# Performance work log

Measured on AMD Instinct MI355X. Metric: run time of the kernel, lower is better.

Reference implementation:

```python
import jax, jax.numpy as jnp
import numpy as np

B, S, H = 8, 1024, 1024
NH, HD = 16, 64
LN_EPS = 1e-12


def setup_inputs() -> dict:
    key = jax.random.key(0)
    ks = jax.random.split(key, 8)
    sd = 0.02
    return {
        "hidden_states": jax.random.normal(ks[0], (B, S, H), jnp.float32),
        "attention_mask": jnp.zeros((B, 1, 1, S), jnp.float32),
        "Wq": jax.random.normal(ks[1], (H, H), jnp.float32) * sd,
        "bq": jnp.zeros((H,), jnp.float32),
        "Wk": jax.random.normal(ks[2], (H, H), jnp.float32) * sd,
        "bk": jnp.zeros((H,), jnp.float32),
        "Wv": jax.random.normal(ks[3], (H, H), jnp.float32) * sd,
        "bv": jnp.zeros((H,), jnp.float32),
        "Wo": jax.random.normal(ks[4], (H, H), jnp.float32) * sd,
        "bo": jnp.zeros((H,), jnp.float32),
        "ln_gamma": jnp.ones((H,), jnp.float32),
        "ln_beta": jnp.zeros((H,), jnp.float32),
    }


def _heads(x):
    # [B,S,H] -> [B,NH,S,HD]
    return x.reshape(B, S, NH, HD).transpose(0, 2, 1, 3)


def reference(hidden_states, attention_mask, Wq, bq, Wk, bk, Wv, bv, Wo, bo, ln_gamma, ln_beta):
    # QKV projections (torch Linear: x @ W.T + b)
    q = _heads(hidden_states @ Wq.T + bq)
    k = _heads(hidden_states @ Wk.T + bk)
    v = _heads(hidden_states @ Wv.T + bv)
    # scaled dot-product attention with additive mask
    scores = jnp.einsum("bhqd,bhkd->bhqk", q, k) / np.sqrt(HD).astype(np.float32)
    scores = scores + attention_mask  # broadcast [B,1,1,S]
    probs = jax.nn.softmax(scores, axis=-1)
    ctx = jnp.einsum("bhqk,bhkd->bhqd", probs, v)
    ctx = ctx.transpose(0, 2, 1, 3).reshape(B, S, H)
    # output projection + residual + LayerNorm
    out = ctx @ Wo.T + bo
    x = out + hidden_states
    mu = jnp.mean(x, axis=-1, keepdims=True)
    var = jnp.var(x, axis=-1, keepdims=True)
    return (x - mu) * jax.lax.rsqrt(var + LN_EPS) * ln_gamma + ln_beta
```

## Files before the change

kernel.cpp:

```cpp
#include <hip/hip_runtime.h>
#include <stdint.h>

typedef __attribute__((ext_vector_type(8))) __bf16 bf16x8;
typedef __attribute__((ext_vector_type(8))) unsigned short ushortx8;
typedef __attribute__((ext_vector_type(4))) unsigned short ushortx4;
typedef __attribute__((ext_vector_type(4))) short short4v;
typedef __attribute__((ext_vector_type(4))) float floatx4;

#define LOG2E 1.4426950408889634f
#define QSCALE 0.18033688011112043f

#define ASYNC16(g, l) __builtin_amdgcn_global_load_lds( \
    (__attribute__((address_space(1))) void*)(g),       \
    (__attribute__((address_space(3))) void*)(l), 16, 0, 0)

__device__ __forceinline__ unsigned short f2bf(float f) {
    unsigned int u = __float_as_uint(f);
    u += 0x7fffu + ((u >> 16) & 1u);
    return (unsigned short)(u >> 16);
}
__device__ __forceinline__ float bf2f(unsigned short u) {
    return __uint_as_float((unsigned)u << 16);
}

__device__ __forceinline__ floatx4 mfma32(bf16x8 a, bf16x8 b, floatx4 c) {
    return __builtin_amdgcn_mfma_f32_16x16x32_bf16(a, b, c, 0, 0, 0);
}
__device__ __forceinline__ floatx4 mfma16(short4v a, short4v b, floatx4 c) {
    return __builtin_amdgcn_mfma_f32_16x16x16bf16_1k(a, b, c, 0, 0, 0);
}

__global__ __launch_bounds__(256) void cvt_all(
    const float* __restrict__ hidden,
    const float* __restrict__ Wq, const float* __restrict__ Wk,
    const float* __restrict__ Wv, const float* __restrict__ Wo,
    unsigned short* __restrict__ hid_bf,
    unsigned short* __restrict__ oqkv, unsigned short* __restrict__ oo)
{
    const float* src;
    unsigned short* dst;
    int i;
    if (blockIdx.x < 4096) {
        src = hidden; dst = hid_bf;
        i = blockIdx.x * 256 + threadIdx.x;
    } else {
        int blk = (blockIdx.x - 4096) >> 9;
        src = (blk == 0) ? Wq : (blk == 1) ? Wk : (blk == 2) ? Wv : Wo;
        dst = (blk == 3) ? oo : oqkv + (size_t)blk * 1048576;
        i = ((blockIdx.x - 4096) & 511) * 256 + threadIdx.x;
    }
    const float4* p = (const float4*)src + (size_t)i * 2;
    float4 a = p[0], b = p[1];
    ushortx8 o;
    o[0] = f2bf(a.x); o[1] = f2bf(a.y); o[2] = f2bf(a.z); o[3] = f2bf(a.w);
    o[4] = f2bf(b.x); o[5] = f2bf(b.y); o[6] = f2bf(b.z); o[7] = f2bf(b.w);
    *((ushortx8*)dst + i) = o;
}

template<bool SWAP>
__device__ __forceinline__ void kloop_bk64(
    const unsigned short* __restrict__ Ag,
    const unsigned short* __restrict__ Wg,
    unsigned short* As, unsigned short* Bs,
    int wm, int wn, int l16, int quad, int t,
    floatx4 acc[4][4])
{
#pragma unroll 1
    for (int k0 = 0; k0 < 1024; k0 += 64) {
        __syncthreads();
#pragma unroll
        for (int i = 0; i < 4; i++) {
            ASYNC16(Ag + (size_t)i * 32 * 1024 + k0, As + i * 2048 + t * 8);
            ASYNC16(Wg + (size_t)i * 32 * 1024 + k0, Bs + i * 2048 + t * 8);
        }
        __syncthreads();
#pragma unroll
        for (int s = 0; s < 2; s++) {
            int pb = ((s * 4 + quad) ^ (l16 & 7)) * 8;
            bf16x8 af[4], bfr[4];
#pragma unroll
            for (int mt = 0; mt < 4; mt++)
                af[mt] = *(const bf16x8*)(As + (wm + mt * 16 + l16) * 64 + pb);
#pragma unroll
            for (int nt = 0; nt < 4; nt++)
                bfr[nt] = *(const bf16x8*)(Bs + (wn + nt * 16 + l16) * 64 + pb);
            if (SWAP) {
#pragma unroll
                for (int ft = 0; ft < 4; ft++)
#pragma unroll
                    for (int st = 0; st < 4; st++)
                        acc[ft][st] = mfma32(bfr[ft], af[st], acc[ft][st]);
            } else {
#pragma unroll
                for (int mt = 0; mt < 4; mt++)
#pragma unroll
                    for (int nt = 0; nt < 4; nt++)
                        acc[mt][nt] = mfma32(af[mt], bfr[nt], acc[mt][nt]);
            }
        }
    }
}

__global__ __launch_bounds__(256) void gemm_qkv(
    const unsigned short* __restrict__ A,
    const unsigned short* __restrict__ W,
    const float* __restrict__ bq, const float* __restrict__ bk, const float* __restrict__ bv,
    unsigned short* __restrict__ Qo, unsigned short* __restrict__ Ko,
    unsigned short* __restrict__ Vo)
{
    __shared__ unsigned short As[128 * 64];
    __shared__ unsigned short Bs[128 * 64];
    const int t = threadIdx.x;
    const int wave = t >> 6, lane = t & 63;
    const int quad = lane >> 4, l16 = lane & 15;
    const int wm = (wave >> 1) * 64, wn = (wave & 1) * 64;
    const int srow = t >> 3;
    const int scol = ((t & 7) ^ (srow & 7)) * 8;

    const unsigned short* Ag = A + ((size_t)blockIdx.x * 128 + srow) * 1024 + scol;
    const unsigned short* Wg = W + ((size_t)blockIdx.y * 128 + srow) * 1024 + scol;

    floatx4 acc[4][4] = {};
    kloop_bk64<true>(Ag, Wg, As, Bs, wm, wn, l16, quad, t, acc);

    int y = blockIdx.y;
    if (y < 16) {
        const float* bp = (y < 8) ? bq : bk;
        unsigned short* op = (y < 8) ? Qo : Ko;
        float sc = (y < 8) ? QSCALE : 1.0f;
#pragma unroll
        for (int ft = 0; ft < 4; ft++) {
            int featg = (y * 128 + wn + ft * 16 + quad * 4) & 1023;
            float4 b4 = *(const float4*)(bp + featg);
            int h = featg >> 6, d = featg & 63;
#pragma unroll
            for (int st = 0; st < 4; st++) {
                int sg = blockIdx.x * 128 + wm + st * 16 + l16;
                int b = sg >> 10, s = sg & 1023;
                ushortx4 o4;
                o4[0] = f2bf((acc[ft][st][0] + b4.x) * sc);
                o4[1] = f2bf((acc[ft][st][1] + b4.y) * sc);
                o4[2] = f2bf((acc[ft][st][2] + b4.z) * sc);
                o4[3] = f2bf((acc[ft][st][3] + b4.w) * sc);
                *(ushortx4*)(op + (((size_t)(b * 16 + h) * 1024 + s) * 64 + d)) = o4;
            }
        }
    } else {
#pragma unroll
        for (int ft = 0; ft < 4; ft++) {
            int featg = (y * 128 + wn + ft * 16 + quad * 4) & 1023;
            float4 b4 = *(const float4*)(bv + featg);
#pragma unroll
            for (int r = 0; r < 4; r++) {
                int feat = featg + r;
                int h = feat >> 6, d = feat & 63;
                float bias = (r == 0) ? b4.x : (r == 1) ? b4.y : (r == 2) ? b4.z : b4.w;
#pragma unroll
                for (int st = 0; st < 4; st++) {
                    int sg = blockIdx.x * 128 + wm + st * 16 + l16;
                    int b = sg >> 10, s = sg & 1023;
                    int sp = (s & ~63) + (st >> 1) * 32 + (l16 >> 2) * 8 + (st & 1) * 4 + (l16 & 3);
                    Vo[((size_t)(b * 16 + h) * 64 + d) * 1024 + sp] = f2bf(acc[ft][st][r] + bias);
                }
            }
        }
    }
}

__global__ __launch_bounds__(256) void attn(
    const unsigned short* __restrict__ Q,
    const unsigned short* __restrict__ Kg,
    const unsigned short* __restrict__ Vt,
    const float* __restrict__ mask,
    unsigned short* __restrict__ ctx)
{
    __shared__ unsigned short Ks[64 * 64];
    __shared__ unsigned short Vs[64 * 64];
    __shared__ float Msall[1024];

    const int t = threadIdx.x;
    const int wave = t >> 6, lane = t & 63, quad = lane >> 4, l16 = lane & 15;
    const int s7 = l16 & 7;
    const int head = blockIdx.x;
    const int b = head >> 4, h = head & 15;
    const int q0 = blockIdx.y * 128;
    const unsigned short* Qh = Q + (size_t)head * 65536;
    const unsigned short* Kh = Kg + (size_t)head * 65536;
    const unsigned short* Vh = Vt + (size_t)head * 65536;

    const int srow = t >> 3;
    const int scol = ((t & 7) ^ (srow & 7)) * 8;

    {
        float4 m4 = *(const float4*)(mask + b * 1024 + t * 4);
        m4.x *= LOG2E; m4.y *= LOG2E; m4.z *= LOG2E; m4.w *= LOG2E;
        *(float4*)(Msall + t * 4) = m4;
    }

    bf16x8 qf[2][2];
#pragma unroll
    for (int qg = 0; qg < 2; qg++) {
        const unsigned short* qp = Qh + (size_t)(q0 + wave * 32 + qg * 16 + l16) * 64 + quad * 8;
        qf[qg][0] = *(const bf16x8*)(qp);
        qf[qg][1] = *(const bf16x8*)(qp + 32);
    }

    float rs0 = 0.f, rs1 = 0.f;
    floatx4 o_acc[2][4] = {};

    for (int k0 = 0; k0 < 1024; k0 += 64) {
        __syncthreads();
#pragma unroll
        for (int i = 0; i < 2; i++) {
            ASYNC16(Kh + (size_t)(k0 + i * 32 + srow) * 64 + scol, Ks + i * 2048 + t * 8);
            ASYNC16(Vh + (size_t)(i * 32 + srow) * 1024 + k0 + scol, Vs + i * 2048 + t * 8);
        }
        __syncthreads();

        short4v pf0[4], pf1[4];
#pragma unroll
        for (int nt = 0; nt < 4; nt++) {
            int krow = nt * 16 + l16;
            bf16x8 kf0 = *(const bf16x8*)(Ks + krow * 64 + ((quad ^ s7) * 8));
            bf16x8 kf1 = *(const bf16x8*)(Ks + krow * 64 + (((4 + quad) ^ s7) * 8));
            floatx4 mk = *(const floatx4*)(Msall + k0 + nt * 16 + quad * 4);
            floatx4 z0 = {0.f, 0.f, 0.f, 0.f};
            z0 = mfma32(kf0, qf[0][0], z0);
            z0 = mfma32(kf1, qf[0][1], z0);
            floatx4 z1 = {0.f, 0.f, 0.f, 0.f};
            z1 = mfma32(kf0, qf[1][0], z1);
            z1 = mfma32(kf1, qf[1][1], z1);
#pragma unroll
            for (int r = 0; r < 4; r++) {
                float p0 = exp2f(z0[r] + mk[r]);
                float p1 = exp2f(z1[r] + mk[r]);
                rs0 += p0;
                rs1 += p1;
                pf0[nt][r] = (short)(__float_as_uint(p0) >> 16);
                pf1[nt][r] = (short)(__float_as_uint(p1) >> 16);
            }
        }

#pragma unroll
        for (int dt = 0; dt < 4; dt++) {
            int vrow = dt * 16 + l16;
            ushortx8 v01 = *(const ushortx8*)(Vs + vrow * 64 + ((quad ^ s7) * 8));
            ushortx8 v23 = *(const ushortx8*)(Vs + vrow * 64 + (((4 + quad) ^ s7) * 8));
            short4v vf0 = {(short)v01[0], (short)v01[1], (short)v01[2], (short)v01[3]};
            short4v vf1 = {(short)v01[4], (short)v01[5], (short)v01[6], (short)v01[7]};
            short4v vf2 = {(short)v23[0], (short)v23[1], (short)v23[2], (short)v23[3]};
            short4v vf3 = {(short)v23[4], (short)v23[5], (short)v23[6], (short)v23[7]};
            o_acc[0][dt] = mfma16(vf0, pf0[0], o_acc[0][dt]);
            o_acc[0][dt] = mfma16(vf1, pf0[1], o_acc[0][dt]);
            o_acc[0][dt] = mfma16(vf2, pf0[2], o_acc[0][dt]);
            o_acc[0][dt] = mfma16(vf3, pf0[3], o_acc[0][dt]);
            o_acc[1][dt] = mfma16(vf0, pf1[0], o_acc[1][dt]);
            o_acc[1][dt] = mfma16(vf1, pf1[1], o_acc[1][dt]);
            o_acc[1][dt] = mfma16(vf2, pf1[2], o_acc[1][dt]);
            o_acc[1][dt] = mfma16(vf3, pf1[3], o_acc[1][dt]);
        }
    }

#pragma unroll
    for (int qg = 0; qg < 2; qg++) {
        float v = (qg == 0) ? rs0 : rs1;
        v += __shfl_xor(v, 16);
        v += __shfl_xor(v, 32);
        float inv_l = 1.0f / v;
        int qrow = q0 + wave * 32 + qg * 16 + l16;
#pragma unroll
        for (int dt = 0; dt < 4; dt++) {
            ushortx4 o4;
#pragma unroll
            for (int r = 0; r < 4; r++) o4[r] = f2bf(o_acc[qg][dt][r] * inv_l);
            *(ushortx4*)(ctx + ((size_t)(b * 1024 + qrow)) * 1024 + h * 64 + dt * 16 + quad * 4) = o4;
        }
    }
}

__global__ __launch_bounds__(256) void gemm_proj(
    const unsigned short* __restrict__ A,
    const unsigned short* __restrict__ W,
    const float* __restrict__ bo,
    const unsigned short* __restrict__ resid,
    unsigned short* __restrict__ X)
{
    __shared__ unsigned short As[128 * 64];
    __shared__ unsigned short Bs[128 * 64];
    const int t = threadIdx.x;
    const int wave = t >> 6, lane = t & 63;
    const int quad = lane >> 4, l16 = lane & 15;
    const int wm = (wave >> 1) * 64, wn = (wave & 1) * 64;
    const int srow = t >> 3;
    const int scol = ((t & 7) ^ (srow & 7)) * 8;

    const unsigned short* Ag = A + ((size_t)blockIdx.x * 128 + srow) * 1024 + scol;
    const unsigned short* Wg = W + ((size_t)blockIdx.y * 128 + srow) * 1024 + scol;

    floatx4 acc[4][4] = {};
    kloop_bk64<false>(Ag, Wg, As, Bs, wm, wn, l16, quad, t, acc);

#pragma unroll
    for (int nt = 0; nt < 4; nt++) {
        int gn = blockIdx.y * 128 + wn + nt * 16 + l16;
        float bias = bo[gn];
#pragma unroll
        for (int mt = 0; mt < 4; mt++) {
#pragma unroll
            for (int r = 0; r < 4; r++) {
                int gm = blockIdx.x * 128 + wm + mt * 16 + quad * 4 + r;
                size_t off = (size_t)gm * 1024 + gn;
                X[off] = f2bf(acc[mt][nt][r] + bias + bf2f(resid[off]));
            }
        }
    }
}

__global__ __launch_bounds__(256) void ln_k(const unsigned short* __restrict__ X,
                                            const float* __restrict__ g,
                                            const float* __restrict__ be,
                                            float* __restrict__ out)
{
    int row = blockIdx.x;
    int t = threadIdx.x;
    const unsigned short* xr = X + (size_t)row * 1024;
    ushortx4 xb = *(const ushortx4*)(xr + t * 4);
    float4 v;
    v.x = bf2f(xb[0]);
    v.y = bf2f(xb[1]);
    v.z = bf2f(xb[2]);
    v.w = bf2f(xb[3]);
    float s = v.x + v.y + v.z + v.w;
    float ss = v.x * v.x + v.y * v.y + v.z * v.z + v.w * v.w;
    for (int off = 1; off < 64; off <<= 1) {
        s += __shfl_xor(s, off);
        ss += __shfl_xor(ss, off);
    }
    __shared__ float red[8];
    int wave = t >> 6, lane = t & 63;
    if (lane == 0) { red[wave] = s; red[4 + wave] = ss; }
    __syncthreads();
    s = red[0] + red[1] + red[2] + red[3];
    ss = red[4] + red[5] + red[6] + red[7];
    float mu = s * (1.f / 1024.f);
    float var = ss * (1.f / 1024.f) - mu * mu;
    float inv = rsqrtf(var + 1e-12f);
    float4 gv = *(const float4*)(g + t * 4);
    float4 bv = *(const float4*)(be + t * 4);
    float4 o;
    o.x = (v.x - mu) * inv * gv.x + bv.x;
    o.y = (v.y - mu) * inv * gv.y + bv.y;
    o.z = (v.z - mu) * inv * gv.z + bv.z;
    o.w = (v.w - mu) * inv * gv.w + bv.w;
    *(float4*)(out + (size_t)row * 1024 + t * 4) = o;
}

extern "C" void kernel_launch(void* const* d_in, const int* in_sizes, int n_in,
                              void* d_out, int out_size, void* d_ws, size_t ws_size,
                              hipStream_t stream)
{
    const float* hidden = (const float*)d_in[0];
    const float* mask   = (const float*)d_in[1];
    const float* Wq = (const float*)d_in[2];
    const float* bq = (const float*)d_in[3];
    const float* Wk = (const float*)d_in[4];
    const float* bk = (const float*)d_in[5];
    const float* Wv = (const float*)d_in[6];
    const float* bv = (const float*)d_in[7];
    const float* Wo = (const float*)d_in[8];
    const float* bo = (const float*)d_in[9];
    const float* gamma = (const float*)d_in[10];
    const float* beta  = (const float*)d_in[11];
    float* out = (float*)d_out;

    char* ws = (char*)d_ws;
    unsigned short* hid_bf  = (unsigned short*)(ws + 0);
    unsigned short* wqkv_bf = (unsigned short*)(ws + 16777216);
    unsigned short* wo_bf   = (unsigned short*)(ws + 23068672);
    unsigned short* vt_bf   = (unsigned short*)(ws + 25165824);
    unsigned short* ctx_bf  = (unsigned short*)(ws + 41943040);
    unsigned short* q_bf    = (unsigned short*)(ws + 58720256);
    unsigned short* k_bf    = (unsigned short*)(ws + 75497472);
    unsigned short* x_bf    = (unsigned short*)(ws + 58720256);

    cvt_all<<<6144, 256, 0, stream>>>(hidden, Wq, Wk, Wv, Wo, hid_bf, wqkv_bf, wo_bf);

    gemm_qkv<<<dim3(64, 24), 256, 0, stream>>>(hid_bf, wqkv_bf, bq, bk, bv, q_bf, k_bf, vt_bf);
    attn<<<dim3(128, 8), 256, 0, stream>>>(q_bf, k_bf, vt_bf, mask, ctx_bf);
    gemm_proj<<<dim3(64, 8), 256, 0, stream>>>(ctx_bf, wo_bf, bo, hid_bf, x_bf);
    ln_k<<<8192, 256, 0, stream>>>(x_bf, gamma, beta, out);
}
```

Before: 274.5 us.

## Rewrite QKV GEMM with 256x256 tiles, 8 waves, double-buffered async LDS pipeline

The QKV projection kernel moves from 128x128 tiles with 4 waves to 256x256 tiles with 8 waves of 512 threads. It double-buffers A and B in LDS and staggers async global-to-LDS loads two k-steps ahead across the compute phases. Explicit waitcnt, barrier and setprio calls aim to overlap memory with MFMA work and raise arithmetic intensity per block. The cost is 128KB of LDS per block and only 384 blocks, which risks low occupancy and a wave-quantization tail across the CUs.

```diff
diff --git a/kernel.cpp b/kernel.cpp
--- a/kernel.cpp
+++ b/kernel.cpp
@@ -101,42 +101,126 @@
     }
 }
 
-__global__ __launch_bounds__(256) void gemm_qkv(
+__global__ __launch_bounds__(512, 2) void gemm_qkv(
     const unsigned short* __restrict__ A,
     const unsigned short* __restrict__ W,
     const float* __restrict__ bq, const float* __restrict__ bk, const float* __restrict__ bv,
     unsigned short* __restrict__ Qo, unsigned short* __restrict__ Ko,
     unsigned short* __restrict__ Vo)
 {
-    __shared__ unsigned short As[128 * 64];
-    __shared__ unsigned short Bs[128 * 64];
+    __shared__ unsigned short As[2][16384];
+    __shared__ unsigned short Bs[2][16384];
     const int t = threadIdx.x;
-    const int wave = t >> 6, lane = t & 63;
-    const int quad = lane >> 4, l16 = lane & 15;
-    const int wm = (wave >> 1) * 64, wn = (wave & 1) * 64;
-    const int srow = t >> 3;
-    const int scol = ((t & 7) ^ (srow & 7)) * 8;
-
-    const unsigned short* Ag = A + ((size_t)blockIdx.x * 128 + srow) * 1024 + scol;
-    const unsigned short* Wg = W + ((size_t)blockIdx.y * 128 + srow) * 1024 + scol;
-
-    floatx4 acc[4][4] = {};
-    kloop_bk64<true>(Ag, Wg, As, Bs, wm, wn, l16, quad, t, acc);
-
-    int y = blockIdx.y;
-    if (y < 16) {
-        const float* bp = (y < 8) ? bq : bk;
-        unsigned short* op = (y < 8) ? Qo : Ko;
-        float sc = (y < 8) ? QSCALE : 1.0f;
-#pragma unroll
-        for (int ft = 0; ft < 4; ft++) {
-            int featg = (y * 128 + wn + ft * 16 + quad * 4) & 1023;
-            float4 b4 = *(const float4*)(bp + featg);
-            int h = featg >> 6, d = featg & 63;
-#pragma unroll
-            for (int st = 0; st < 4; st++) {
-                int sg = blockIdx.x * 128 + wm + st * 16 + l16;
-                int b = sg >> 10, s = sg & 1023;
+    const int lane = t & 63, quad = lane >> 4, l16 = lane & 15;
+    const int wid = t >> 6;
+    const int wm = (wid >> 2) * 128;
+    const int wn = (wid & 3) * 64;
+    const int rr = t >> 3;
+    const int cc = ((t & 7) ^ (rr & 7)) * 8;
+    const int t8 = t * 8;
+
+    const unsigned short* Ab = A + ((size_t)blockIdx.x * 256 + rr) * 1024 + cc;
+    const unsigned short* Wb = W + ((size_t)blockIdx.y * 256 + rr) * 1024 + cc;
+
+#define SA(bf_, u_, kt_) ASYNC16(Ab + (size_t)(u_) * 65536 + (kt_) * 64, &As[bf_][(u_) * 4096 + t8])
+#define SB(bf_, u_, kt_) ASYNC16(Wb + (size_t)(u_) * 65536 + (kt_) * 64, &Bs[bf_][(u_) * 4096 + t8])
+
+    SA(0, 0, 0); SA(0, 1, 0); SA(0, 2, 0); SA(0, 3, 0);
+    SB(0, 0, 0); SB(0, 1, 0); SB(0, 2, 0); SB(0, 3, 0);
+    SB(1, 0, 1); SB(1, 1, 1); SA(1, 0, 1); SA(1, 2, 1); SB(1, 2, 1); SB(1, 3, 1);
+    asm volatile("s_waitcnt vmcnt(6)" ::: "memory");
+    __builtin_amdgcn_s_barrier();
+
+    floatx4 acc[4][8] = {};
+
+#pragma unroll 1
+    for (int kt = 0; kt < 16; ++kt) {
+        const int cur = kt & 1, nb = cur ^ 1;
+        const unsigned short* Ac = As[cur];
+        const unsigned short* Bc = Bs[cur];
+        bf16x8 bfr[4][2];
+
+        {
+            bf16x8 a0[2][2];
+#pragma unroll
+            for (int j = 0; j < 2; ++j)
+#pragma unroll
+                for (int s = 0; s < 2; ++s)
+                    a0[j][s] = *(const bf16x8*)(Ac + (wm + j * 16 + l16) * 64 +
+                                                ((s * 4 + quad) ^ (l16 & 7)) * 8);
+#pragma unroll
+            for (int ft = 0; ft < 4; ++ft)
+#pragma unroll
+                for (int s = 0; s < 2; ++s)
+                    bfr[ft][s] = *(const bf16x8*)(Bc + (wn + ft * 16 + l16) * 64 +
+                                                  ((s * 4 + quad) ^ (l16 & 7)) * 8);
+            if (kt < 15) { SA(nb, 1, kt + 1); SA(nb, 3, kt + 1); }
+            __builtin_amdgcn_s_barrier();
+            asm volatile("s_waitcnt lgkmcnt(0)" ::: "memory");
+            __builtin_amdgcn_sched_barrier(0);
+            __builtin_amdgcn_s_setprio(1);
+#pragma unroll
+            for (int ft = 0; ft < 4; ++ft)
+#pragma unroll
+                for (int j = 0; j < 2; ++j) {
+                    acc[ft][j] = mfma32(bfr[ft][0], a0[j][0], acc[ft][j]);
+                    acc[ft][j] = mfma32(bfr[ft][1], a0[j][1], acc[ft][j]);
+                }
+            __builtin_amdgcn_s_setprio(0);
+            __builtin_amdgcn_s_barrier();
+        }
+#pragma unroll
+        for (int p = 1; p < 4; ++p) {
+            bf16x8 a0[2][2];
+#pragma unroll
+            for (int j = 0; j < 2; ++j)
+#pragma unroll
+                for (int s = 0; s < 2; ++s)
+                    a0[j][s] = *(const bf16x8*)(Ac + (wm + (p * 2 + j) * 16 + l16) * 64 +
+                                                ((s * 4 + quad) ^ (l16 & 7)) * 8);
+            if (kt < 14) {
+                if (p == 1)      { SB(cur, 0, kt + 2); SB(cur, 1, kt + 2); }
+                else if (p == 2) { SA(cur, 0, kt + 2); SA(cur, 2, kt + 2); }
+                else             { SB(cur, 2, kt + 2); SB(cur, 3, kt + 2); }
+            }
+            __builtin_amdgcn_s_barrier();
+            asm volatile("s_waitcnt lgkmcnt(0)" ::: "memory");
+            __builtin_amdgcn_sched_barrier(0);
+            __builtin_amdgcn_s_setprio(1);
+#pragma unroll
+            for (int ft = 0; ft < 4; ++ft)
+#pragma unroll
+                for (int j = 0; j < 2; ++j) {
+                    acc[ft][p * 2 + j] = mfma32(bfr[ft][0], a0[j][0], acc[ft][p * 2 + j]);
+                    acc[ft][p * 2 + j] = mfma32(bfr[ft][1], a0[j][1], acc[ft][p * 2 + j]);
+                }
+            __builtin_amdgcn_s_setprio(0);
+            if (p < 3) {
+                __builtin_amdgcn_s_barrier();
+            } else {
+                if (kt < 14)       { asm volatile("s_waitcnt vmcnt(6)" ::: "memory"); }
+                else if (kt == 14) { asm volatile("s_waitcnt vmcnt(0)" ::: "memory"); }
+                if (kt < 15) __builtin_amdgcn_s_barrier();
+            }
+        }
+    }
+#undef SA
+#undef SB
+
+    const int y = blockIdx.y;
+    if (y < 8) {
+        const float* bp = (y < 4) ? bq : bk;
+        unsigned short* op = (y < 4) ? Qo : Ko;
+        const float sc = (y < 4) ? QSCALE : 1.0f;
+#pragma unroll
+        for (int ft = 0; ft < 4; ++ft) {
+            const int featg = (y & 3) * 256 + wn + ft * 16 + quad * 4;
+            const float4 b4 = *(const float4*)(bp + featg);
+            const int h = featg >> 6, d = featg & 63;
+#pragma unroll
+            for (int st = 0; st < 8; ++st) {
+                const int sg = blockIdx.x * 256 + wm + st * 16 + l16;
+                const int b = sg >> 10, s = sg & 1023;
                 ushortx4 o4;
                 o4[0] = f2bf((acc[ft][st][0] + b4.x) * sc);
                 o4[1] = f2bf((acc[ft][st][1] + b4.y) * sc);
@@ -147,19 +231,20 @@
         }
     } else {
 #pragma unroll
-        for (int ft = 0; ft < 4; ft++) {
-            int featg = (y * 128 + wn + ft * 16 + quad * 4) & 1023;
-            float4 b4 = *(const float4*)(bv + featg);
-#pragma unroll
-            for (int r = 0; r < 4; r++) {
-                int feat = featg + r;
-                int h = feat >> 6, d = feat & 63;
-                float bias = (r == 0) ? b4.x : (r == 1) ? b4.y : (r == 2) ? b4.z : b4.w;
-#pragma unroll
-                for (int st = 0; st < 4; st++) {
-                    int sg = blockIdx.x * 128 + wm + st * 16 + l16;
-                    int b = sg >> 10, s = sg & 1023;
-                    int sp = (s & ~63) + (st >> 1) * 32 + (l16 >> 2) * 8 + (st & 1) * 4 + (l16 & 3);
+        for (int ft = 0; ft < 4; ++ft) {
+            const int featg = (y & 3) * 256 + wn + ft * 16 + quad * 4;
+            const float4 b4 = *(const float4*)(bv + featg);
+#pragma unroll
+            for (int r = 0; r < 4; ++r) {
+                const int feat = featg + r;
+                const int h = feat >> 6, d = feat & 63;
+                const float bias = (r == 0) ? b4.x : (r == 1) ? b4.y : (r == 2) ? b4.z : b4.w;
+#pragma unroll
+                for (int st = 0; st < 8; ++st) {
+                    const int sg = blockIdx.x * 256 + wm + st * 16 + l16;
+                    const int b = sg >> 10, s = sg & 1023;
+                    const int sp = (s & ~63) + ((st >> 1) & 1) * 32 + (l16 >> 2) * 8 +
+                                   (st & 1) * 4 + (l16 & 3);
                     Vo[((size_t)(b * 16 + h) * 64 + d) * 1024 + sp] = f2bf(acc[ft][st][r] + bias);
                 }
             }
@@ -385,7 +470,7 @@
 
     cvt_all<<<6144, 256, 0, stream>>>(hidden, Wq, Wk, Wv, Wo, hid_bf, wqkv_bf, wo_bf);
 
-    gemm_qkv<<<dim3(64, 24), 256, 0, stream>>>(hid_bf, wqkv_bf, bq, bk, bv, q_bf, k_bf, vt_bf);
+    gemm_qkv<<<dim3(32, 12), 512, 0, stream>>>(hid_bf, wqkv_bf, bq, bk, bv, q_bf, k_bf, vt_bf);
     attn<<<dim3(128, 8), 256, 0, stream>>>(q_bf, k_bf, vt_bf, mask, ctx_bf);
     gemm_proj<<<dim3(64, 8), 256, 0, stream>>>(ctx_bf, wo_bf, bo, hid_bf, x_bf);
     ln_k<<<8192, 256, 0, stream>>>(x_bf, gamma, beta, out);
```

After: 272.7 us. About the same (-0.6%).
